# Kernel tuning notes

Hardware: AMD Instinct MI355X
Metric: run time of the kernel (lower is better)

Reference implementation:

```python
import jax, jax.numpy as jnp
import numpy as np

B, L, N, CIN = 16, 12, 2048, 3
EMB, GRAP, LAYERS, OUT = 64, 16, 3, 12
SP, TID, DIW = 16, 16, 16
M = EMB + SP + TID + DIW  # model_size = 112


def setup_inputs() -> dict:
    key = jax.random.key(0)
    ks = jax.random.split(key, 12)
    s = jnp.float32(0.02)
    return {
        "history_data": jax.random.uniform(ks[0], (B, L, N, CIN), dtype=jnp.float32),
        "adj": jax.nn.softmax(jax.random.normal(ks[1], (N, N), dtype=jnp.float32), axis=1),
        "node_emb": jax.random.normal(ks[2], (N, SP), dtype=jnp.float32) * s,
        "tid_emb": jax.random.normal(ks[3], (288, TID), dtype=jnp.float32) * s,
        "diw_emb": jax.random.normal(ks[4], (7, DIW), dtype=jnp.float32) * s,
        "W_in": jax.random.normal(ks[5], (CIN, EMB), dtype=jnp.float32) * s,
        "b_in": jnp.zeros((EMB,), jnp.float32),
        "W_pre": jax.random.normal(ks[6], (M, 4 * M), dtype=jnp.float32) * s,
        "b_pre": jnp.zeros((4 * M,), jnp.float32),
        "E_dy": jax.random.normal(ks[7], (N, GRAP), dtype=jnp.float32) * s,
        "W_dy": jax.random.normal(ks[8], (M, 4 * M), dtype=jnp.float32) * s,
        "b_dy": jnp.zeros((4 * M,), jnp.float32),
        "W_dec": jax.random.normal(ks[9], (OUT, LAYERS, M), dtype=jnp.float32) * s,
        "b_dec": jnp.zeros((OUT,), jnp.float32),
        "W_out": jax.random.normal(ks[10], (OUT, OUT), dtype=jnp.float32) * s,
        "b_out": jnp.zeros((OUT,), jnp.float32),
    }


def _run_layer(hidd_t, A, W, b):
    """Graph-conv LSTM-style recurrent layer; returns last-timestep hidden [B,N,M]."""
    def step(ct, x):  # x: [B,N,M]
        xa = jnp.einsum('bkm,nk->bnm', x, A)      # adjacency message passing
        gates = xa @ W + b                         # [B,N,4M]
        i, f, g, o = jnp.split(gates, 4, axis=-1)
        ct = jax.nn.sigmoid(f) * ct + jax.nn.sigmoid(i) * jnp.tanh(g)
        ht = jax.nn.sigmoid(o) * jnp.tanh(ct)
        return ct, ht
    ct0 = jnp.zeros(hidd_t.shape[1:], hidd_t.dtype)  # [B,N,M]
    _, hts = jax.lax.scan(step, ct0, hidd_t)
    return hts[-1]


def reference(history_data, adj, node_emb, tid_emb, diw_emb, W_in, b_in,
              W_pre, b_pre, E_dy, W_dy, b_dy, W_dec, b_dec, W_out, b_out):
    Bx, Lx = history_data.shape[0], history_data.shape[1]
    # temporal embedding indices (truncating cast, matches torch LongTensor)
    t_idx = (history_data[..., 1] * 288).astype(jnp.int32)
    d_idx = (history_data[..., 2] * 7).astype(jnp.int32)
    inp = history_data @ W_in + b_in                                   # [B,L,N,EMB]
    node = jnp.broadcast_to(node_emb, (Bx, Lx) + node_emb.shape)       # [B,L,N,SP]
    hidd = jnp.concatenate([inp, node, tid_emb[t_idx], diw_emb[d_idx]], axis=-1)  # [B,L,N,M]
    hidd_t = jnp.moveaxis(hidd, 1, 0)                                  # [L,B,N,M]
    A_dy = jax.nn.softmax(jax.nn.relu(E_dy @ E_dy.T), axis=1)          # adaptive adjacency
    outs = [_run_layer(hidd_t, adj, W_pre, b_pre)]                     # layer 0: predefined graph
    for _ in range(LAYERS - 1):
        outs.append(_run_layer(hidd_t, A_dy, W_dy, b_dy))              # layers >0: dynamic graph
    final = jnp.stack(outs, axis=1)                                    # [B,LAYERS,N,M]
    # decoder Conv2d(layer_num->out_len, kernel (1,M)) then 1x1 Conv2d
    x = jnp.einsum('bznm,ozm->bon', final, W_dec) + b_dec[None, :, None]
    x = jnp.einsum('bon,po->bpn', x, W_out) + b_out[None, :, None]
    return x  # [B,OUT,N]
```

## Files before the change

kernel.cpp:

```cpp
#include <hip/hip_runtime.h>
#include <hip/hip_bf16.h>
#include <cstdint>
#include <cstddef>

typedef float f4 __attribute__((ext_vector_type(4)));
typedef short s16x8 __attribute__((ext_vector_type(8)));
typedef short s16x4 __attribute__((ext_vector_type(4)));

#define N_NODES 2048
#define BATCH 16
#define LSEQ 12
#define MDIM 112
#define GDIM 448
#define KC 35
#define NCOLS_X 6784
#define NREAL (KC*BATCH*LSEQ)
#define NA_HI 6720
#define NA_LO 6736
#define RS_COL 6752
#define XROW 7680
#define KBIG 2048
#define KL 64
#define WTB_SH (GDIM * KL)

#define GLDS16(SRC, DST)                                                        \
    __builtin_amdgcn_global_load_lds(                                           \
        (const __attribute__((address_space(1))) void*)(SRC),                   \
        (__attribute__((address_space(3))) void*)(DST), 16, 0, 0)

#define MFMA16(ACC, AV, BV) \
    ACC = __builtin_amdgcn_mfma_f32_16x16x32_bf16(AV, BV, ACC, 0, 0, 0)

__device__ __forceinline__ short bf16hi(float v) {
    union { __hip_bfloat16 h; short s; } u;
    u.h = __float2bfloat16(v);
    return u.s;
}
__device__ __forceinline__ short bf16lo(float v) {
    union { __hip_bfloat16 h; short s; } u;
    u.h = __float2bfloat16(v);
    float r = v - __bfloat162float(u.h);
    u.h = __float2bfloat16(r);
    return u.s;
}
__device__ __forceinline__ float rcpf_(float x)  { return __builtin_amdgcn_rcpf(x); }
__device__ __forceinline__ float sigf_(float x)  { return rcpf_(1.0f + __expf(-x)); }
__device__ __forceinline__ float tanhf_(float x) { return 1.0f - 2.0f * rcpf_(1.0f + __expf(2.0f * x)); }

__global__ void adaptive_adj_kernel(const float* __restrict__ E,
                                    __hip_bfloat16* __restrict__ Abig)
{
    __shared__ float sbuf[N_NODES];
    __shared__ float red[256];
    const int n = blockIdx.x;
    const int tid = threadIdx.x;
    float en[16];
#pragma unroll
    for (int i = 0; i < 16; ++i) en[i] = E[n * 16 + i];
    float lmax = -3.4e38f;
    for (int k = tid; k < N_NODES; k += 256) {
        const float* ek = E + k * 16;
        float d = 0.f;
#pragma unroll
        for (int i = 0; i < 16; ++i) d += en[i] * ek[i];
        d = fmaxf(d, 0.0f);
        sbuf[k] = d;
        lmax = fmaxf(lmax, d);
    }
    red[tid] = lmax; __syncthreads();
    for (int s = 128; s > 0; s >>= 1) {
        if (tid < s) red[tid] = fmaxf(red[tid], red[tid + s]);
        __syncthreads();
    }
    float mx = red[0];
    __syncthreads();
    float lsum = 0.f;
    for (int k = tid; k < N_NODES; k += 256) {
        float e = __expf(sbuf[k] - mx);
        sbuf[k] = e;
        lsum += e;
    }
    red[tid] = lsum; __syncthreads();
    for (int s = 128; s > 0; s >>= 1) {
        if (tid < s) red[tid] += red[tid + s];
        __syncthreads();
    }
    float rinv = rcpf_(red[0]);
    __syncthreads();

    __hip_bfloat16* arow = Abig + (size_t)(2048 + n) * KBIG;
    for (int k = tid; k < N_NODES; k += 256)
        arow[k] = __float2bfloat16(sbuf[k] * rinv);
}

__global__ void wtb_pack_kernel(const float* __restrict__ W_in,
                                const float* __restrict__ b_in,
                                const float* __restrict__ Wp,
                                const float* __restrict__ bp,
                                const float* __restrict__ Wd,
                                const float* __restrict__ bd,
                                short* __restrict__ outp)
{
    int idx = blockIdx.x * 256 + threadIdx.x;
    if (idx >= 2 * GDIM * KL) return;
    int z = idx >= GDIM * KL;
    int rem = idx - z * GDIM * KL;
    const float* W  = z ? Wd : Wp;
    const float* bg = z ? bd : bp;
    int p = rem & 63;
    int r = rem >> 6;
    int tile = r >> 4, gc = r & 15;
    int mi = tile >> 2, co = tile & 3;
    int g = co * 112 + mi * 16 + gc;

    float v = 0.f; bool lo = false; bool zero = false;
    #define DOTW(VEC) ({ float s_ = 0.f;                                     \
        for (int m = 0; m < 64; ++m) s_ += (VEC)[m] * W[(size_t)m * GDIM + g];\
        s_; })
    if (p < 3)         v = DOTW(W_in + p * 64);
    else if (p < 35)   v = W[(size_t)(80 + p - 3) * GDIM + g];
    else if (p < 38)   v = DOTW(W_in + (p - 35) * 64);
    else if (p < 41) { v = DOTW(W_in + (p - 38) * 64); lo = true; }
    else if (p == 41)  v = bg[g];
    else if (p == 42)  v = DOTW(b_in);
    else if (p < 59)   v = W[(size_t)(64 + p - 43) * GDIM + g];
    else if (p == 59) { v = bg[g]; lo = true; }
    else if (p == 60) { v = DOTW(b_in); lo = true; }
    else zero = true;
    #undef DOTW
    short s = zero ? (short)0 : (lo ? bf16lo(v) : bf16hi(v));
    int a = r * 128 + p * 2;
    int asw = a ^ (((a >> 7) & 7) << 4);
    outp[(size_t)z * WTB_SH + (asw >> 1)] = s;
}

#define AQUADS (2048 * 2048 / 4)
#define XQUADS (NCOLS_X * 2048 / 4)
__global__ void pack_build_kernel(const float* __restrict__ adj,
                                  const float* __restrict__ hist,
                                  const float* __restrict__ tid_emb,
                                  const float* __restrict__ diw_emb,
                                  const float* __restrict__ node_emb,
                                  __hip_bfloat16* __restrict__ Abig,
                                  __hip_bfloat16* __restrict__ XT)
{
    int idx = blockIdx.x * 256 + threadIdx.x;
    if (idx < AQUADS) {
        int e0 = idx << 2;
        int k = e0 & 2047;
        int m = e0 >> 11;
        f4 v = *(const f4*)(adj + (size_t)m * 2048 + k);
        s16x4 o = { bf16hi(v[0]), bf16hi(v[1]), bf16hi(v[2]), bf16hi(v[3]) };
        *(s16x4*)((short*)Abig + (size_t)m * KBIG + k) = o;
        return;
    }
    int xi = idx - AQUADS;
    if (xi >= XQUADS) return;
    int e0 = xi << 2;
    int k0 = e0 & 2047;
    int jl = e0 >> 11;
    s16x4 o = {0, 0, 0, 0};
    if (jl < NREAL) {
        int c = jl % KC;
        int bl = jl / KC;
#pragma unroll
        for (int i = 0; i < 4; ++i) {
            const float* h = hist + ((size_t)(bl * N_NODES + k0 + i)) * 3;
            float v;
            if (c < 3) v = h[c];
            else if (c < 19) { int ti = (int)(h[1] * 288.0f); v = tid_emb[ti * 16 + (c - 3)]; }
            else             { int di = (int)(h[2] * 7.0f);   v = diw_emb[di * 16 + (c - 19)]; }
            o[i] = bf16hi(v);
        }
    } else if (jl >= NA_HI && jl < NA_LO) {
        int e = jl - NA_HI;
#pragma unroll
        for (int i = 0; i < 4; ++i) o[i] = bf16hi(node_emb[(k0 + i) * 16 + e]);
    } else if (jl >= NA_LO && jl < RS_COL) {
        int e = jl - NA_LO;
#pragma unroll
        for (int i = 0; i < 4; ++i) o[i] = bf16lo(node_emb[(k0 + i) * 16 + e]);
    } else if (jl == RS_COL) {
        short one = bf16hi(1.0f);
        o[0] = one; o[1] = one; o[2] = one; o[3] = one;
    }
    *(s16x4*)((short*)XT + (size_t)jl * KBIG + k0) = o;
}

__global__ __launch_bounds__(512, 4) void gemm_bf16_kernel(const short* __restrict__ A,
                                                           const short* __restrict__ BT,
                                                           short* __restrict__ XAhi,
                                                           float* __restrict__ na_pre,
                                                           float* __restrict__ na_dy,
                                                           float* __restrict__ rs_pre,
                                                           float* __restrict__ rs_dy)
{
    __shared__ short As[256 * 64];
    __shared__ short Bs[128 * 64];
    const int tid = threadIdx.x;
    const int w = tid >> 6;
    const int l = tid & 63;
    const int wr = w >> 1;
    const int wc = w & 1;
    const int lm = l & 15;

    const int bid = blockIdx.y * 53 + blockIdx.x;
    const int sid = (bid & 7) * 106 + (bid >> 3);
    const int col = sid >> 4;
    const int row = sid & 15;
    const int m0 = row * 256;
    const int jt = col * 128;

    const int srow = tid >> 3;
    const int koct = (tid & 7) ^ (srow & 7);
    const size_t gA = (size_t)(m0 + srow) * KBIG + koct * 8;
    const size_t gB = (size_t)(jt + srow) * KBIG + koct * 8;
    char* lA = (char*)As + srow * 128 + (tid & 7) * 16;
    char* lB = (char*)Bs + srow * 128 + (tid & 7) * 16;

    f4 acc[4][4];
#pragma unroll
    for (int i = 0; i < 4; ++i)
#pragma unroll
        for (int j = 0; j < 4; ++j)
#pragma unroll
            for (int e = 0; e < 4; ++e) acc[i][j][e] = 0.f;

    const int sm  = (l & 7) << 4;
    const int k16 = (l >> 4) * 16;

    for (int kt = 0; kt < KBIG; kt += 64) {
        __syncthreads();
        GLDS16(A  + gA + kt,                      lA);
        GLDS16(A  + gA + kt + (size_t)64  * KBIG, lA + 64  * 128);
        GLDS16(A  + gA + kt + (size_t)128 * KBIG, lA + 128 * 128);
        GLDS16(A  + gA + kt + (size_t)192 * KBIG, lA + 192 * 128);
        GLDS16(BT + gB + kt,                      lB);
        GLDS16(BT + gB + kt + (size_t)64  * KBIG, lB + 64  * 128);
        __syncthreads();
#pragma unroll
        for (int ks = 0; ks < 2; ++ks) {
            const int ko = (ks * 64 + k16) ^ sm;
            s16x8 a[4], b[4];
#pragma unroll
            for (int mi = 0; mi < 4; ++mi)
                a[mi] = *(const s16x8*)((const char*)As + (wr * 64 + mi * 16 + lm) * 128 + ko);
#pragma unroll
            for (int ni = 0; ni < 4; ++ni)
                b[ni] = *(const s16x8*)((const char*)Bs + (wc * 64 + ni * 16 + lm) * 128 + ko);
#pragma unroll
            for (int mi = 0; mi < 4; ++mi)
#pragma unroll
                for (int ni = 0; ni < 4; ++ni)
                    MFMA16(acc[mi][ni], a[mi], b[ni]);
        }
    }

    const int rbase = m0 + wr * 64 + (l >> 4) * 4;
    const int cbase = jt + wc * 64 + lm;
#pragma unroll
    for (int mi = 0; mi < 4; ++mi)
#pragma unroll
        for (int ni = 0; ni < 4; ++ni) {
            int cc = cbase + ni * 16;
            if (cc < NREAL) {
                int bt = cc / KC;
                int c  = cc - bt * KC;
#pragma unroll
                for (int reg = 0; reg < 4; ++reg) {
                    size_t roff = (size_t)(rbase + mi * 16 + reg) * XROW;
                    float v = acc[mi][ni][reg];
                    XAhi[roff + (size_t)bt * 40 + c] = bf16hi(v);
                    if (c < 3) XAhi[roff + (size_t)bt * 40 + 36 + c] = bf16lo(v);
                }
            }
        }

    if (jt == 6656 && wc == 1) {
#pragma unroll
        for (int mi = 0; mi < 4; ++mi)
#pragma unroll
            for (int reg = 0; reg < 4; ++reg) {
                int r = rbase + mi * 16 + reg;
                float nav = acc[mi][0][reg] + acc[mi][1][reg];
                int rr = r & 2047;
                if (r < 2048) {
                    na_pre[rr * 16 + lm] = nav;
                    if (lm == 0) rs_pre[rr] = acc[mi][2][reg];
                } else {
                    na_dy[rr * 16 + lm] = nav;
                    if (lm == 0) rs_dy[rr] = acc[mi][2][reg];
                }
            }
    }
}

__global__ __launch_bounds__(512, 4) void lstm6_kernel(
    const short* __restrict__ XAhi,
    const short* __restrict__ WtBg,
    const float* __restrict__ na_pre, const float* __restrict__ na_dy,
    const float* __restrict__ rs_pre, const float* __restrict__ rs_dy,
    float* __restrict__ H)
{
    __shared__ short sWtb[WTB_SH];
    __shared__ short sXa[128 * KL];
    const int tid = threadIdx.x;
    const int w = tid >> 6, l = tid & 63;
    const int n0 = blockIdx.x * 128;
    const int b  = blockIdx.y;
    const int z  = blockIdx.z;
    const float* na = z ? na_dy : na_pre;
    const float* rs = z ? rs_dy : rs_pre;

    {
        const char* gW = (const char*)(WtBg + (size_t)z * WTB_SH);
        char* lW = (char*)sWtb;
        for (int it = 0; it < 7; ++it) {
            int base = (it * 8 + w) * 64;
            GLDS16(gW + (size_t)(base + l) * 16, lW + base * 16);
        }
    }

    const int sr = tid & 127;
    const int pp = tid >> 7;
    const short* xarow = XAhi + (size_t)(z * 2048 + n0 + sr) * XROW;
    const float* narow = na + (size_t)(n0 + sr) * 16;
    const float rsv = rs[n0 + sr];
    char* wrow = (char*)sXa + sr * 128;
    const int wswz = (sr & 7) << 4;

    const int lm = l & 15;
    const int sm = (l & 7) << 4;
    const int kof0 = ((l >> 4) * 16) ^ sm;
    const int kof1 = (64 + (l >> 4) * 16) ^ sm;
    const int an = w * 16 + lm;
    const char* xab = (const char*)sXa;
    const char* wtbb = (const char*)sWtb;
    float* Hout = H + (size_t)z * BATCH * N_NODES * MDIM;

    float cc[7][4];
#pragma unroll
    for (int mi = 0; mi < 7; ++mi)
#pragma unroll
        for (int q = 0; q < 4; ++q) cc[mi][q] = 0.f;

    s16x8 ph0 = {0,0,0,0,0,0,0,0}, ph1 = ph0;
    s16x4 p0 = {0,0,0,0}, p32 = p0, plo = p0;
    {
        const int bt = b * LSEQ;
        if (pp < 2) {
            ph0 = *(const s16x8*)(xarow + bt * 40 + pp * 16);
            ph1 = *(const s16x8*)(xarow + bt * 40 + pp * 16 + 8);
        } else if (pp == 2) {
            p0  = *(const s16x4*)(xarow + bt * 40);
            p32 = *(const s16x4*)(xarow + bt * 40 + 32);
            plo = *(const s16x4*)(xarow + bt * 40 + 36);
        }
    }

    for (int t = 0; t < LSEQ; ++t) {
        __syncthreads();
        if (pp < 2) {
            *(s16x8*)(wrow + ((pp * 32 + 0)  ^ wswz)) = ph0;
            *(s16x8*)(wrow + ((pp * 32 + 16) ^ wswz)) = ph1;
        } else if (pp == 2) {
            short v[16];
            v[0] = p32[0]; v[1] = p32[1]; v[2] = p32[2];
            v[3] = plo[0]; v[4] = plo[1]; v[5] = plo[2];
            v[6] = p0[0];  v[7] = p0[1];  v[8] = p0[2];
            v[9]  = bf16hi(1.0f);
            v[10] = bf16hi(rsv);
#pragma unroll
            for (int j = 11; j < 16; ++j) v[j] = bf16hi(narow[j - 11]);
#pragma unroll
            for (int q = 0; q < 4; ++q) {
                s16x4 sv = { v[q * 4], v[q * 4 + 1], v[q * 4 + 2], v[q * 4 + 3] };
                *(s16x4*)(wrow + ((2 * 32 + q * 8) ^ wswz)) = sv;
            }
        } else {
            short v[16];
#pragma unroll
            for (int j = 0; j < 11; ++j) v[j] = bf16hi(narow[5 + j]);
            v[11] = bf16hi(1.0f);
            v[12] = bf16hi(rsv);
            v[13] = 0; v[14] = 0; v[15] = 0;
#pragma unroll
            for (int q = 0; q < 4; ++q) {
                s16x4 sv = { v[q * 4], v[q * 4 + 1], v[q * 4 + 2], v[q * 4 + 3] };
                *(s16x4*)(wrow + ((3 * 32 + q * 8) ^ wswz)) = sv;
            }
        }
        __syncthreads();

        if (t + 1 < LSEQ) {
            const int bt = b * LSEQ + t + 1;
            if (pp < 2) {
                ph0 = *(const s16x8*)(xarow + bt * 40 + pp * 16);
                ph1 = *(const s16x8*)(xarow + bt * 40 + pp * 16 + 8);
            } else if (pp == 2) {
                p0  = *(const s16x4*)(xarow + bt * 40);
                p32 = *(const s16x4*)(xarow + bt * 40 + 32);
                plo = *(const s16x4*)(xarow + bt * 40 + 36);
            }
        }

        s16x8 a0 = *(const s16x8*)(xab + an * 128 + kof0);
        s16x8 a1 = *(const s16x8*)(xab + an * 128 + kof1);
#pragma unroll
        for (int mi = 0; mi < 7; ++mi) {
            const char* bb = wtbb + (mi * 64 + lm) * 128;
            f4 gi = {0.f, 0.f, 0.f, 0.f};
            f4 gf = gi, gg = gi;
            MFMA16(gi, a0, *(const s16x8*)(bb + kof0));
            MFMA16(gi, a1, *(const s16x8*)(bb + kof1));
            MFMA16(gf, a0, *(const s16x8*)(bb + 2048 + kof0));
            MFMA16(gf, a1, *(const s16x8*)(bb + 2048 + kof1));
            MFMA16(gg, a0, *(const s16x8*)(bb + 4096 + kof0));
            MFMA16(gg, a1, *(const s16x8*)(bb + 4096 + kof1));
#pragma unroll
            for (int q = 0; q < 4; ++q) {
                float si = sigf_(gi[q]);
                float sf = sigf_(gf[q]);
                float tg = tanhf_(gg[q]);
                cc[mi][q] = sf * cc[mi][q] + si * tg;
            }
            if (t == LSEQ - 1) {
                f4 go = {0.f, 0.f, 0.f, 0.f};
                MFMA16(go, a0, *(const s16x8*)(bb + 6144 + kof0));
                MFMA16(go, a1, *(const s16x8*)(bb + 6144 + kof1));
#pragma unroll
                for (int q = 0; q < 4; ++q) {
                    float h = sigf_(go[q]) * tanhf_(cc[mi][q]);
                    Hout[((size_t)b * N_NODES + n0 + w * 16 + (l >> 4) * 4 + q) * MDIM
                         + mi * 16 + lm] = h;
                }
            }
        }
    }
}

__global__ void decode_kernel(const float* __restrict__ H,
                              const float* __restrict__ Wdec,
                              const float* __restrict__ bdec,
                              const float* __restrict__ Wout,
                              const float* __restrict__ bout,
                              float* __restrict__ out)
{
    int g = blockIdx.x * 256 + threadIdx.x;
    if (g >= BATCH * N_NODES) return;
    int b = g >> 11;
    int n = g & 2047;
    const f4* h0 = (const f4*)(H + (size_t)g * MDIM);
    const f4* h1 = (const f4*)(H + (size_t)BATCH * N_NODES * MDIM + (size_t)g * MDIM);
    float x[12];
#pragma unroll
    for (int o = 0; o < 12; ++o) x[o] = bdec[o];
    for (int mq = 0; mq < 28; ++mq) {
        f4 a0 = h0[mq], a1 = h1[mq];
#pragma unroll
        for (int e = 0; e < 4; ++e) {
            int m = mq * 4 + e;
#pragma unroll
            for (int o = 0; o < 12; ++o)
                x[o] += a0[e] * Wdec[(o * 3 + 0) * MDIM + m]
                      + a1[e] * (Wdec[(o * 3 + 1) * MDIM + m] + Wdec[(o * 3 + 2) * MDIM + m]);
        }
    }
#pragma unroll
    for (int p = 0; p < 12; ++p) {
        float s = bout[p];
#pragma unroll
        for (int o = 0; o < 12; ++o) s += Wout[p * 12 + o] * x[o];
        out[((size_t)b * 12 + p) * N_NODES + n] = s;
    }
}

extern "C" void kernel_launch(void* const* d_in, const int* in_sizes, int n_in,
                              void* d_out, int out_size, void* d_ws, size_t ws_size,
                              hipStream_t stream)
{
    const float* hist   = (const float*)d_in[0];
    const float* adj    = (const float*)d_in[1];
    const float* node_e = (const float*)d_in[2];
    const float* tid_e  = (const float*)d_in[3];
    const float* diw_e  = (const float*)d_in[4];
    const float* W_in   = (const float*)d_in[5];
    const float* b_in   = (const float*)d_in[6];
    const float* W_pre  = (const float*)d_in[7];
    const float* b_pre  = (const float*)d_in[8];
    const float* E_dy   = (const float*)d_in[9];
    const float* W_dy   = (const float*)d_in[10];
    const float* b_dy   = (const float*)d_in[11];
    const float* W_dec  = (const float*)d_in[12];
    const float* b_dec  = (const float*)d_in[13];
    const float* W_out  = (const float*)d_in[14];
    const float* b_out  = (const float*)d_in[15];
    float* out = (float*)d_out;

    float* ws = (float*)d_ws;
    const size_t XAHI_F = (size_t)4096 * XROW / 2;
    const size_t ABIG_F = (size_t)4096 * KBIG / 2;
    const size_t XT_F   = (size_t)NCOLS_X * KBIG / 2;

    short* XAhi  = (short*)ws;
    float* AbigF = ws + XAHI_F;
    __hip_bfloat16* Abig = (__hip_bfloat16*)AbigF;
    float* H     = AbigF;
    __hip_bfloat16* XTc = (__hip_bfloat16*)(ws + XAHI_F + ABIG_F);
    float* tail = ws + XAHI_F + ABIG_F + XT_F;
    float* na_pre = tail;                     tail += (size_t)N_NODES * 16;
    float* na_dy  = tail;                     tail += (size_t)N_NODES * 16;
    float* rs_pre = tail;                     tail += N_NODES;
    float* rs_dy  = tail;                     tail += N_NODES;
    short* WtBg   = (short*)tail;

    adaptive_adj_kernel<<<N_NODES, 256, 0, stream>>>(E_dy, Abig);
    wtb_pack_kernel<<<(2 * GDIM * KL + 255) / 256, 256, 0, stream>>>(
        W_in, b_in, W_pre, b_pre, W_dy, b_dy, WtBg);

    pack_build_kernel<<<(AQUADS + XQUADS + 255) / 256, 256, 0, stream>>>(
        adj, hist, tid_e, diw_e, node_e, Abig, XTc);

    gemm_bf16_kernel<<<dim3(53, 16), 512, 0, stream>>>(
        (const short*)Abig, (const short*)XTc, XAhi, na_pre, na_dy, rs_pre, rs_dy);

    lstm6_kernel<<<dim3(N_NODES / 128, BATCH, 2), 512, 0, stream>>>(
        XAhi, WtBg, na_pre, na_dy, rs_pre, rs_dy, H);

    decode_kernel<<<(BATCH * N_NODES + 255) / 256, 256, 0, stream>>>(
        H, W_dec, b_dec, W_out, b_out, out);
}
```

Measured before the change: 283.2 us.

## Store GEMM output in MFMA fragment layout and load LSTM operands directly

The GEMM epilogue now writes the message-passed activations into a per-block, per-timestep slot layout (48 shorts per node) that matches the MFMA A-operand fragment. The LSTM kernel then loads its operands straight from global memory into registers and keeps the constant node-embedding and row-sum columns in registers. This removes the shared-memory staging buffer and the two barriers per timestep. The cost is scattered, strided stores in the GEMM epilogue and an extra duplicated hi copy of the first three columns.

```diff
diff --git a/kernel.cpp b/kernel.cpp
--- a/kernel.cpp
+++ b/kernel.cpp
@@ -18,7 +18,7 @@
 #define NA_HI 6720
 #define NA_LO 6736
 #define RS_COL 6752
-#define XROW 7680
+#define FSLOT 48
 #define KBIG 2048
 #define KL 64
 #define WTB_SH (GDIM * KL)
@@ -189,7 +189,7 @@
 
 __global__ __launch_bounds__(512, 4) void gemm_bf16_kernel(const short* __restrict__ A,
                                                            const short* __restrict__ BT,
-                                                           short* __restrict__ XAhi,
+                                                           short* __restrict__ XAfrag,
                                                            float* __restrict__ na_pre,
                                                            float* __restrict__ na_dy,
                                                            float* __restrict__ rs_pre,
@@ -268,10 +268,15 @@
                 int c  = cc - bt * KC;
 #pragma unroll
                 for (int reg = 0; reg < 4; ++reg) {
-                    size_t roff = (size_t)(rbase + mi * 16 + reg) * XROW;
+                    int r = rbase + mi * 16 + reg;
+                    size_t fr = (((size_t)(r >> 7) * 192 + bt) * 128 + (r & 127)) * FSLOT;
                     float v = acc[mi][ni][reg];
-                    XAhi[roff + (size_t)bt * 40 + c] = bf16hi(v);
-                    if (c < 3) XAhi[roff + (size_t)bt * 40 + 36 + c] = bf16lo(v);
+                    short hv = bf16hi(v);
+                    XAfrag[fr + c] = hv;
+                    if (c < 3) {
+                        XAfrag[fr + 35 + c] = bf16lo(v);
+                        XAfrag[fr + 38 + c] = hv;
+                    }
                 }
             }
         }
@@ -295,18 +300,17 @@
     }
 }
 
-__global__ __launch_bounds__(512, 4) void lstm6_kernel(
-    const short* __restrict__ XAhi,
+__global__ __launch_bounds__(512, 4) void lstm7_kernel(
+    const short* __restrict__ XAfrag,
     const short* __restrict__ WtBg,
     const float* __restrict__ na_pre, const float* __restrict__ na_dy,
     const float* __restrict__ rs_pre, const float* __restrict__ rs_dy,
     float* __restrict__ H)
 {
     __shared__ short sWtb[WTB_SH];
-    __shared__ short sXa[128 * KL];
     const int tid = threadIdx.x;
     const int w = tid >> 6, l = tid & 63;
-    const int n0 = blockIdx.x * 128;
+    const int nb = blockIdx.x;
     const int b  = blockIdx.y;
     const int z  = blockIdx.z;
     const float* na = z ? na_dy : na_pre;
@@ -321,20 +325,36 @@
         }
     }
 
-    const int sr = tid & 127;
-    const int pp = tid >> 7;
-    const short* xarow = XAhi + (size_t)(z * 2048 + n0 + sr) * XROW;
-    const float* narow = na + (size_t)(n0 + sr) * 16;
-    const float rsv = rs[n0 + sr];
-    char* wrow = (char*)sXa + sr * 128;
-    const int wswz = (sr & 7) << 4;
-
     const int lm = l & 15;
+    const int gr = l >> 4;
+    const int an = w * 16 + lm;
+    const int gn = nb * 128 + an;
+
+    short cna[16];
+#pragma unroll
+    for (int e = 0; e < 16; ++e) cna[e] = bf16hi(na[gn * 16 + e]);
+    const short c1  = bf16hi(1.0f);
+    const short crs = bf16hi(rs[gn]);
+    s16x8 a1c = {0, 0, 0, 0, 0, 0, 0, 0};
+    if (gr == 1) {
+        a1c[1] = c1; a1c[2] = crs;
+        a1c[3] = cna[0]; a1c[4] = cna[1]; a1c[5] = cna[2];
+        a1c[6] = cna[3]; a1c[7] = cna[4];
+    } else if (gr == 2) {
+        a1c[0] = cna[5];  a1c[1] = cna[6];  a1c[2] = cna[7];  a1c[3] = cna[8];
+        a1c[4] = cna[9];  a1c[5] = cna[10]; a1c[6] = cna[11]; a1c[7] = cna[12];
+    } else if (gr == 3) {
+        a1c[0] = cna[13]; a1c[1] = cna[14]; a1c[2] = cna[15];
+        a1c[3] = c1; a1c[4] = crs;
+    }
+
+    const short* xaf = XAfrag + (((size_t)(z * 16 + nb) * 16 + b) * 12) * (128 * FSLOT)
+                     + an * FSLOT;
+    const int off1 = (gr == 0) ? 32 : 40;
+
     const int sm = (l & 7) << 4;
     const int kof0 = ((l >> 4) * 16) ^ sm;
     const int kof1 = (64 + (l >> 4) * 16) ^ sm;
-    const int an = w * 16 + lm;
-    const char* xab = (const char*)sXa;
     const char* wtbb = (const char*)sWtb;
     float* Hout = H + (size_t)z * BATCH * N_NODES * MDIM;
 
@@ -344,68 +364,23 @@
 #pragma unroll
         for (int q = 0; q < 4; ++q) cc[mi][q] = 0.f;
 
-    s16x8 ph0 = {0,0,0,0,0,0,0,0}, ph1 = ph0;
-    s16x4 p0 = {0,0,0,0}, p32 = p0, plo = p0;
-    {
-        const int bt = b * LSEQ;
-        if (pp < 2) {
-            ph0 = *(const s16x8*)(xarow + bt * 40 + pp * 16);
-            ph1 = *(const s16x8*)(xarow + bt * 40 + pp * 16 + 8);
-        } else if (pp == 2) {
-            p0  = *(const s16x4*)(xarow + bt * 40);
-            p32 = *(const s16x4*)(xarow + bt * 40 + 32);
-            plo = *(const s16x4*)(xarow + bt * 40 + 36);
-        }
-    }
+    s16x8 pa0 = *(const s16x8*)(xaf + gr * 8);
+    s16x8 pL  = *(const s16x8*)(xaf + off1);
+
+    __syncthreads();
 
     for (int t = 0; t < LSEQ; ++t) {
-        __syncthreads();
-        if (pp < 2) {
-            *(s16x8*)(wrow + ((pp * 32 + 0)  ^ wswz)) = ph0;
-            *(s16x8*)(wrow + ((pp * 32 + 16) ^ wswz)) = ph1;
-        } else if (pp == 2) {
-            short v[16];
-            v[0] = p32[0]; v[1] = p32[1]; v[2] = p32[2];
-            v[3] = plo[0]; v[4] = plo[1]; v[5] = plo[2];
-            v[6] = p0[0];  v[7] = p0[1];  v[8] = p0[2];
-            v[9]  = bf16hi(1.0f);
-            v[10] = bf16hi(rsv);
-#pragma unroll
-            for (int j = 11; j < 16; ++j) v[j] = bf16hi(narow[j - 11]);
-#pragma unroll
-            for (int q = 0; q < 4; ++q) {
-                s16x4 sv = { v[q * 4], v[q * 4 + 1], v[q * 4 + 2], v[q * 4 + 3] };
-                *(s16x4*)(wrow + ((2 * 32 + q * 8) ^ wswz)) = sv;
-            }
-        } else {
-            short v[16];
-#pragma unroll
-            for (int j = 0; j < 11; ++j) v[j] = bf16hi(narow[5 + j]);
-            v[11] = bf16hi(1.0f);
-            v[12] = bf16hi(rsv);
-            v[13] = 0; v[14] = 0; v[15] = 0;
-#pragma unroll
-            for (int q = 0; q < 4; ++q) {
-                s16x4 sv = { v[q * 4], v[q * 4 + 1], v[q * 4 + 2], v[q * 4 + 3] };
-                *(s16x4*)(wrow + ((3 * 32 + q * 8) ^ wswz)) = sv;
-            }
-        }
-        __syncthreads();
+        s16x8 a0 = pa0;
+        s16x8 a1;
+        if (gr == 0) a1 = pL;
+        else { a1 = a1c; if (gr == 1) a1[0] = pL[0]; }
 
         if (t + 1 < LSEQ) {
-            const int bt = b * LSEQ + t + 1;
-            if (pp < 2) {
-                ph0 = *(const s16x8*)(xarow + bt * 40 + pp * 16);
-                ph1 = *(const s16x8*)(xarow + bt * 40 + pp * 16 + 8);
-            } else if (pp == 2) {
-                p0  = *(const s16x4*)(xarow + bt * 40);
-                p32 = *(const s16x4*)(xarow + bt * 40 + 32);
-                plo = *(const s16x4*)(xarow + bt * 40 + 36);
-            }
-        }
-
-        s16x8 a0 = *(const s16x8*)(xab + an * 128 + kof0);
-        s16x8 a1 = *(const s16x8*)(xab + an * 128 + kof1);
+            const short* sl = xaf + (size_t)(t + 1) * (128 * FSLOT);
+            pa0 = *(const s16x8*)(sl + gr * 8);
+            pL  = *(const s16x8*)(sl + off1);
+        }
+
 #pragma unroll
         for (int mi = 0; mi < 7; ++mi) {
             const char* bb = wtbb + (mi * 64 + lm) * 128;
@@ -431,7 +406,7 @@
 #pragma unroll
                 for (int q = 0; q < 4; ++q) {
                     float h = sigf_(go[q]) * tanhf_(cc[mi][q]);
-                    Hout[((size_t)b * N_NODES + n0 + w * 16 + (l >> 4) * 4 + q) * MDIM
+                    Hout[((size_t)b * N_NODES + nb * 128 + w * 16 + (l >> 4) * 4 + q) * MDIM
                          + mi * 16 + lm] = h;
                 }
             }
@@ -498,16 +473,16 @@
     float* out = (float*)d_out;
 
     float* ws = (float*)d_ws;
-    const size_t XAHI_F = (size_t)4096 * XROW / 2;
+    const size_t XAF_F  = (size_t)4096 * 192 * FSLOT / 2;
     const size_t ABIG_F = (size_t)4096 * KBIG / 2;
     const size_t XT_F   = (size_t)NCOLS_X * KBIG / 2;
 
-    short* XAhi  = (short*)ws;
-    float* AbigF = ws + XAHI_F;
+    short* XAfrag = (short*)ws;
+    float* AbigF = ws + XAF_F;
     __hip_bfloat16* Abig = (__hip_bfloat16*)AbigF;
     float* H     = AbigF;
-    __hip_bfloat16* XTc = (__hip_bfloat16*)(ws + XAHI_F + ABIG_F);
-    float* tail = ws + XAHI_F + ABIG_F + XT_F;
+    __hip_bfloat16* XTc = (__hip_bfloat16*)(ws + XAF_F + ABIG_F);
+    float* tail = ws + XAF_F + ABIG_F + XT_F;
     float* na_pre = tail;                     tail += (size_t)N_NODES * 16;
     float* na_dy  = tail;                     tail += (size_t)N_NODES * 16;
     float* rs_pre = tail;                     tail += N_NODES;
@@ -522,10 +497,10 @@
         adj, hist, tid_e, diw_e, node_e, Abig, XTc);
 
     gemm_bf16_kernel<<<dim3(53, 16), 512, 0, stream>>>(
-        (const short*)Abig, (const short*)XTc, XAhi, na_pre, na_dy, rs_pre, rs_dy);
-
-    lstm6_kernel<<<dim3(N_NODES / 128, BATCH, 2), 512, 0, stream>>>(
-        XAhi, WtBg, na_pre, na_dy, rs_pre, rs_dy, H);
+        (const short*)Abig, (const short*)XTc, XAfrag, na_pre, na_dy, rs_pre, rs_dy);
+
+    lstm7_kernel<<<dim3(16, BATCH, 2), 512, 0, stream>>>(
+        XAfrag, WtBg, na_pre, na_dy, rs_pre, rs_dy, H);
 
     decode_kernel<<<(BATCH * N_NODES + 255) / 256, 256, 0, stream>>>(
         H, W_dec, b_dec, W_out, b_out, out);
```

New measurement: 425.9 us. 1.5x slower.

## Double-buffer GEMM LDS tiles with K=32 stages and explicit vmcnt waits

Applied to the files above, without the earlier changes.

Reworks the main bf16 GEMM loop into a two-stage software pipeline. Each stage loads a K=32 slice into one of two LDS buffers while the other is consumed, using s_waitcnt vmcnt and raw barriers instead of full syncthreads. MFMA sections are bracketed with s_setprio to favour math issue. This is meant to hide global-to-LDS load latency behind compute, at the cost of more barriers per K and a more fragile manual swizzle and wait-count scheme.

```diff
diff --git a/kernel.cpp b/kernel.cpp
--- a/kernel.cpp
+++ b/kernel.cpp
@@ -195,8 +195,8 @@
                                                            float* __restrict__ rs_pre,
                                                            float* __restrict__ rs_dy)
 {
-    __shared__ short As[256 * 64];
-    __shared__ short Bs[128 * 64];
+    __shared__ short As[2 * 8192];
+    __shared__ short Bs[2 * 4096];
     const int tid = threadIdx.x;
     const int w = tid >> 6;
     const int l = tid & 63;
@@ -211,12 +211,22 @@
     const int m0 = row * 256;
     const int jt = col * 128;
 
-    const int srow = tid >> 3;
-    const int koct = (tid & 7) ^ (srow & 7);
-    const size_t gA = (size_t)(m0 + srow) * KBIG + koct * 8;
-    const size_t gB = (size_t)(jt + srow) * KBIG + koct * 8;
-    char* lA = (char*)As + srow * 128 + (tid & 7) * 16;
-    char* lB = (char*)Bs + srow * 128 + (tid & 7) * 16;
+    const int lrow = tid >> 3;
+    const int es   = tid & 7;
+    const int sp   = es ^ (lrow & 7);
+    const int shalf = sp >> 2;
+    const int skoct = sp & 3;
+    const size_t gA0 = (size_t)(m0 + lrow        + 128 * shalf) * KBIG + skoct * 8;
+    const size_t gA1 = (size_t)(m0 + 64 + lrow   + 128 * shalf) * KBIG + skoct * 8;
+    const size_t gB0 = (size_t)(jt + lrow        +  64 * shalf) * KBIG + skoct * 8;
+    char* lA0 = (char*)As + tid * 16;
+    char* lA1 = (char*)As + 8192 + tid * 16;
+    char* lB0 = (char*)Bs + tid * 16;
+
+#define GSTAGE(BUF, KT)                                               \
+    GLDS16(A  + gA0 + (KT), lA0 + (BUF) * 16384);                     \
+    GLDS16(A  + gA1 + (KT), lA1 + (BUF) * 16384);                     \
+    GLDS16(BT + gB0 + (KT), lB0 + (BUF) * 8192);
 
     f4 acc[4][4];
 #pragma unroll
@@ -226,35 +236,51 @@
 #pragma unroll
             for (int e = 0; e < 4; ++e) acc[i][j][e] = 0.f;
 
-    const int sm  = (l & 7) << 4;
-    const int k16 = (l >> 4) * 16;
-
-    for (int kt = 0; kt < KBIG; kt += 64) {
-        __syncthreads();
-        GLDS16(A  + gA + kt,                      lA);
-        GLDS16(A  + gA + kt + (size_t)64  * KBIG, lA + 64  * 128);
-        GLDS16(A  + gA + kt + (size_t)128 * KBIG, lA + 128 * 128);
-        GLDS16(A  + gA + kt + (size_t)192 * KBIG, lA + 192 * 128);
-        GLDS16(BT + gB + kt,                      lB);
-        GLDS16(BT + gB + kt + (size_t)64  * KBIG, lB + 64  * 128);
-        __syncthreads();
-#pragma unroll
-        for (int ks = 0; ks < 2; ++ks) {
-            const int ko = (ks * 64 + k16) ^ sm;
-            s16x8 a[4], b[4];
-#pragma unroll
-            for (int mi = 0; mi < 4; ++mi)
-                a[mi] = *(const s16x8*)((const char*)As + (wr * 64 + mi * 16 + lm) * 128 + ko);
-#pragma unroll
-            for (int ni = 0; ni < 4; ++ni)
-                b[ni] = *(const s16x8*)((const char*)Bs + (wc * 64 + ni * 16 + lm) * 128 + ko);
-#pragma unroll
-            for (int mi = 0; mi < 4; ++mi)
-#pragma unroll
-                for (int ni = 0; ni < 4; ++ni)
-                    MFMA16(acc[mi][ni], a[mi], b[ni]);
-        }
-    }
+    const int klm  = (lm & 7) << 4;
+    const int aofc = (((wr >> 1) * 64) + ((l >> 4) * 16)) ^ klm;
+    const int bofc = ((wc * 64) + ((l >> 4) * 16)) ^ klm;
+    const int arow0 = (wr & 1) * 64 + lm;
+
+#define GCOMPUTE(BUF)                                                          \
+    {                                                                          \
+        const char* AsB = (const char*)As + (BUF) * 16384;                     \
+        const char* BsB = (const char*)Bs + (BUF) * 8192;                      \
+        s16x8 a[4], b[4];                                                      \
+        _Pragma("unroll")                                                      \
+        for (int mi = 0; mi < 4; ++mi)                                         \
+            a[mi] = *(const s16x8*)(AsB + (arow0 + mi * 16) * 128 + aofc);     \
+        _Pragma("unroll")                                                      \
+        for (int ni = 0; ni < 4; ++ni)                                         \
+            b[ni] = *(const s16x8*)(BsB + (ni * 16 + lm) * 128 + bofc);        \
+        __builtin_amdgcn_s_setprio(1);                                         \
+        _Pragma("unroll")                                                      \
+        for (int mi = 0; mi < 4; ++mi)                                         \
+            _Pragma("unroll")                                                  \
+            for (int ni = 0; ni < 4; ++ni)                                     \
+                MFMA16(acc[mi][ni], a[mi], b[ni]);                             \
+        __builtin_amdgcn_s_setprio(0);                                         \
+    }
+
+    GSTAGE(0, 0)
+    GSTAGE(1, 32)
+    for (int kt = 0; kt < KBIG - 32; kt += 32) {
+        const int buf = (kt >> 5) & 1;
+        asm volatile("s_waitcnt vmcnt(3)" ::: "memory");
+        __builtin_amdgcn_s_barrier();
+        asm volatile("" ::: "memory");
+        GCOMPUTE(buf)
+        asm volatile("" ::: "memory");
+        __builtin_amdgcn_s_barrier();
+        asm volatile("" ::: "memory");
+        if (kt + 64 < KBIG) { GSTAGE(buf, kt + 64) }
+    }
+    asm volatile("s_waitcnt vmcnt(0)" ::: "memory");
+    __builtin_amdgcn_s_barrier();
+    asm volatile("" ::: "memory");
+    GCOMPUTE(1)
+
+#undef GSTAGE
+#undef GCOMPUTE
 
     const int rbase = m0 + wr * 64 + (l >> 4) * 4;
     const int cbase = jt + wc * 64 + lm;
```

After: 303.0 us. 1.07x slower.
